# Kernel optimization log

Hardware: AMD Instinct MI355X
Metric: run time of the kernel (lower is better)

The kernel has to match this reference:

```python
import jax, jax.numpy as jnp
import numpy as np

B, S, D_MODEL, D_K = 4, 4096, 1024, 128
NEG = jnp.float32(-1e30)  # acts as -inf for masking; exp underflows to exactly 0 in fp32


def setup_inputs() -> dict:
    key = jax.random.key(0)
    ks = jax.random.split(key, 8)
    sc = 1.0 / np.sqrt(D_MODEL)
    x = jax.random.normal(ks[0], (B, S, D_MODEL), jnp.float32)
    padding_mask = (jax.random.uniform(ks[1], (B, S)) > 0.05).astype(jnp.float32)
    Wq = jax.random.normal(ks[2], (D_MODEL, D_K), jnp.float32) * sc
    bq = jax.random.normal(ks[3], (D_K,), jnp.float32) * 0.01
    Wk = jax.random.normal(ks[4], (D_MODEL, D_K), jnp.float32) * sc
    bk = jax.random.normal(ks[5], (D_K,), jnp.float32) * 0.01
    Wv = jax.random.normal(ks[6], (D_MODEL, D_K), jnp.float32) * sc
    bv = jax.random.normal(ks[7], (D_K,), jnp.float32) * 0.01
    return {"x": x, "padding_mask": padding_mask, "Wq": Wq, "bq": bq,
            "Wk": Wk, "bk": bk, "Wv": Wv, "bv": bv}


def reference(x, padding_mask, Wq, bq, Wk, bk, Wv, bv):
    # Self-attention path (enc_dec_layer_input is None), masked=True (causal).
    scale = jnp.sqrt(jnp.float32(Wq.shape[-1]))
    Q = x @ Wq + bq  # [B,S,Dk]
    K = x @ Wk + bk
    V = x @ Wv + bv
    scores = jnp.einsum('bqd,bkd->bqk', Q, K) / scale  # [B,S,S]
    # causal mask (torch: triu(1) filled with -inf) AND padding outer-product mask
    causal = jnp.tril(jnp.ones((S, S), dtype=bool))  # True = allowed
    pm = (padding_mask[:, :, None] * padding_mask[:, None, :]) > 0  # [B,S,S]
    allowed = causal[None] & pm
    scores = jnp.where(allowed, scores, NEG)
    attn = jax.nn.softmax(scores, axis=-1)
    # torch: fully-masked query rows give NaN -> nan_to_num -> 0.
    # A query row is dead iff its own token is padded (diagonal is causally allowed).
    row_alive = padding_mask > 0  # [B,S]
    attn = jnp.where(row_alive[:, :, None], attn, 0.0)
    out = jnp.einsum('bqk,bkd->bqd', attn, V)  # [B,S,Dk]
    return out
```

## Files before the change

### kernel.cpp

```cpp
#include <hip/hip_runtime.h>
#include <hip/hip_bf16.h>
#include <cstdint>

typedef __bf16 bf16x8 __attribute__((ext_vector_type(8)));
typedef float f32x4 __attribute__((ext_vector_type(4)));

#define MFMA16(a, b, c) __builtin_amdgcn_mfma_f32_16x16x32_bf16((a), (b), (c), 0, 0, 0)

__device__ __forceinline__ unsigned short f2bf(float f) {
  union { float f; unsigned u; } v; v.f = f;
  unsigned u = v.u;
  u += 0x7fffu + ((u >> 16) & 1u);
  return (unsigned short)(u >> 16);
}
__device__ __forceinline__ unsigned pk2(float a, float b) {
  __hip_bfloat162 h = __float22bfloat162_rn(make_float2(a, b));
  union { __hip_bfloat162 h; unsigned u; } v; v.h = h; return v.u;
}

__global__ __launch_bounds__(256) void convert_w(
    const float* __restrict__ Wq, const float* __restrict__ Wk,
    const float* __restrict__ Wv, unsigned short* __restrict__ wt) {
  int idx = blockIdx.x * 256 + threadIdx.x;
  int m = idx >> 17;
  int rem = idx & 131071;
  int k = rem >> 7;
  int n = rem & 127;
  const float* W = (m == 0) ? Wq : (m == 1) ? Wk : Wv;
  wt[(size_t)m * 131072 + (size_t)n * 1024 + k] = f2bf(W[(size_t)k * 128 + n]);
}

__global__ __launch_bounds__(512) void qkv_fused(
    const float* __restrict__ x, const unsigned short* __restrict__ wt_all,
    const float* __restrict__ bq, const float* __restrict__ bk,
    const float* __restrict__ bv,
    unsigned short* __restrict__ Qg, unsigned short* __restrict__ Kg,
    unsigned short* __restrict__ Vtg) {
  __shared__ unsigned short x_lds[64][40];
  __shared__ unsigned short w_lds[384][40];
  const int tid = threadIdx.x;
  const int lane = tid & 63;
  const int w = tid >> 6;
  const int m0 = blockIdx.x * 64;
  const int rh = w >> 2;
  const int cq = w & 3;
  const int lr = lane & 15;
  const int lk = (lane >> 4) * 8;

  f32x4 acc[2][6];
#pragma unroll
  for (int m = 0; m < 2; ++m)
#pragma unroll
    for (int n = 0; n < 6; ++n) acc[m][n] = (f32x4){0.f, 0.f, 0.f, 0.f};

  const int xr = tid >> 3;
  const int xc = (tid & 7) * 4;
  const float* xbase = x + (size_t)(m0 + xr) * 1024 + xc;
  const int j0 = tid, j1 = tid + 512, j2 = tid + 1024;
  const int wr0 = j0 >> 2, ws0 = (j0 & 3) * 8;
  const int wr1 = j1 >> 2, ws1 = (j1 & 3) * 8;
  const int wr2 = j2 >> 2, ws2 = (j2 & 3) * 8;
  const unsigned short* wp0 = wt_all + (size_t)wr0 * 1024 + ws0;
  const unsigned short* wp1 = wt_all + (size_t)wr1 * 1024 + ws1;
  const unsigned short* wp2 = wt_all + (size_t)wr2 * 1024 + ws2;

  float4 xA, xB;
  uint4 wA0, wA1, wA2, wB0, wB1, wB2;
  {
    xA = *(const float4*)xbase;
    wA0 = *(const uint4*)wp0; wA1 = *(const uint4*)wp1; wA2 = *(const uint4*)wp2;
    xB = *(const float4*)(xbase + 32);
    wB0 = *(const uint4*)(wp0 + 32); wB1 = *(const uint4*)(wp1 + 32); wB2 = *(const uint4*)(wp2 + 32);
  }

#define QKV_STORE(X, W0, W1, W2)                               \
  {                                                            \
    uint2 xw;                                                  \
    xw.x = pk2(X.x, X.y); xw.y = pk2(X.z, X.w);                \
    *(uint2*)&x_lds[xr][xc] = xw;                              \
    *(uint4*)&w_lds[wr0][ws0] = W0;                            \
    *(uint4*)&w_lds[wr1][ws1] = W1;                            \
    *(uint4*)&w_lds[wr2][ws2] = W2;                            \
  }

#define QKV_COMPUTE()                                          \
  {                                                            \
    bf16x8 af0 = *(const bf16x8*)&x_lds[rh * 32 + lr][lk];     \
    bf16x8 af1 = *(const bf16x8*)&x_lds[rh * 32 + 16 + lr][lk];\
    _Pragma("unroll")                                          \
    for (int n = 0; n < 6; ++n) {                              \
      bf16x8 bfv = *(const bf16x8*)&w_lds[cq * 96 + n * 16 + lr][lk]; \
      acc[0][n] = MFMA16(af0, bfv, acc[0][n]);                 \
      acc[1][n] = MFMA16(af1, bfv, acc[1][n]);                 \
    }                                                          \
  }

  for (int k0 = 0; k0 < 1024; k0 += 64) {
    __syncthreads();
    QKV_STORE(xA, wA0, wA1, wA2);
    __syncthreads();
    if (k0 + 64 < 1024) {
      xA = *(const float4*)(xbase + k0 + 64);
      wA0 = *(const uint4*)(wp0 + k0 + 64);
      wA1 = *(const uint4*)(wp1 + k0 + 64);
      wA2 = *(const uint4*)(wp2 + k0 + 64);
    }
    QKV_COMPUTE();
    __syncthreads();
    QKV_STORE(xB, wB0, wB1, wB2);
    __syncthreads();
    if (k0 + 96 < 1024) {
      xB = *(const float4*)(xbase + k0 + 96);
      wB0 = *(const uint4*)(wp0 + k0 + 96);
      wB1 = *(const uint4*)(wp1 + k0 + 96);
      wB2 = *(const uint4*)(wp2 + k0 + 96);
    }
    QKV_COMPUTE();
  }
#undef QKV_STORE
#undef QKV_COMPUTE

#pragma unroll
  for (int n = 0; n < 6; ++n) {
    const int gcol = cq * 96 + n * 16 + lr;
    const int mode = gcol >> 7;
    const int col = gcol & 127;
    const float bias = (mode == 0) ? bq[col] : (mode == 1) ? bk[col] : bv[col];
#pragma unroll
    for (int m = 0; m < 2; ++m)
#pragma unroll
      for (int r = 0; r < 4; ++r) {
        const int grow = m0 + rh * 32 + m * 16 + (lane >> 4) * 4 + r;
        float val = acc[m][n][r] + bias;
        if (mode == 0) {
          val *= 0.08838834764831845f;
          Qg[(size_t)grow * 128 + col] = f2bf(val);
        } else if (mode == 1) {
          Kg[(size_t)grow * 128 + col] = f2bf(val);
        } else {
          const int bb = grow >> 12, s = grow & 4095;
          Vtg[((size_t)bb * 128 + col) * 4096 + s] = f2bf(val);
        }
      }
  }
}

struct AttnLds {
  union {
    unsigned short K_lds[64][136];
    unsigned short P_lds[4][16][68];
  } u;
  unsigned short V_lds[128][72];
};

__device__ __forceinline__ void attn_tiles(
    AttnLds& S, const unsigned short* __restrict__ Kb,
    const unsigned short* __restrict__ Vb, const float* __restrict__ pmb,
    int q0, int tstart, int tend,
    const bf16x8 (&qf)[4], float& mrow, float& lsum, f32x4 (&o)[8]) {
  const int tid = threadIdx.x;
  const int lane = tid & 63;
  const int w = tid >> 6;
  const int lr = lane & 15;
  const int lg = lane >> 4;
  const int lk = lg * 8;
  const int q_own = q0 + w * 16 + lr;

  for (int t = tstart; t < tend; ++t) {
    const int k0 = t * 64;
    __syncthreads();
    {
      int kr = tid >> 2, seg = (tid & 3) * 32;
      const uint4* src = (const uint4*)(Kb + (size_t)(k0 + kr) * 128 + seg);
      uint4 v0 = src[0], v1 = src[1], v2 = src[2], v3 = src[3];
      uint4* dst = (uint4*)&S.u.K_lds[kr][seg];
      dst[0] = v0; dst[1] = v1; dst[2] = v2; dst[3] = v3;
      int d = tid >> 1, half = (tid & 1) * 32;
      const uint4* vs = (const uint4*)(Vb + (size_t)d * 4096 + k0 + half);
      uint4 u0 = vs[0], u1 = vs[1], u2 = vs[2], u3 = vs[3];
      uint4* vdst = (uint4*)&S.V_lds[d][half];
      vdst[0] = u0; vdst[1] = u1; vdst[2] = u2; vdst[3] = u3;
    }
    __syncthreads();

    f32x4 st[4];
#pragma unroll
    for (int f = 0; f < 4; ++f) {
      st[f] = (f32x4){0.f, 0.f, 0.f, 0.f};
#pragma unroll
      for (int dc = 0; dc < 4; ++dc) {
        bf16x8 kf = *(const bf16x8*)&S.u.K_lds[f * 16 + lr][dc * 32 + lk];
        st[f] = MFMA16(kf, qf[dc], st[f]);
      }
    }

    const unsigned long long mb = __ballot(pmb[k0 + lane] > 0.f);
    unsigned nib[4];
#pragma unroll
    for (int f = 0; f < 4; ++f) nib[f] = (unsigned)(mb >> (16 * f + 4 * lg)) & 0xFu;

    __syncthreads();

    float mx = -1e30f;
    if (k0 + 63 > q0 + (w << 4)) {
#pragma unroll
      for (int f = 0; f < 4; ++f)
#pragma unroll
        for (int r = 0; r < 4; ++r) {
          const bool ok = (((nib[f] >> r) & 1u) != 0u) &&
                          (k0 + 16 * f + 4 * lg + r <= q_own);
          const float s = ok ? st[f][r] : -1e30f;
          st[f][r] = s;
          mx = fmaxf(mx, s);
        }
    } else {
#pragma unroll
      for (int f = 0; f < 4; ++f)
#pragma unroll
        for (int r = 0; r < 4; ++r) {
          const bool ok = ((nib[f] >> r) & 1u) != 0u;
          const float s = ok ? st[f][r] : -1e30f;
          st[f][r] = s;
          mx = fmaxf(mx, s);
        }
    }
    mx = fmaxf(mx, __shfl_xor(mx, 16));
    mx = fmaxf(mx, __shfl_xor(mx, 32));
    const float mnew = fmaxf(mrow, mx);
    const float alpha = __expf(mrow - mnew);
    mrow = mnew;

    float sum = 0.f;
#pragma unroll
    for (int f = 0; f < 4; ++f) {
      const float p0 = (st[f][0] < -1e29f) ? 0.f : __expf(st[f][0] - mnew);
      const float p1 = (st[f][1] < -1e29f) ? 0.f : __expf(st[f][1] - mnew);
      const float p2 = (st[f][2] < -1e29f) ? 0.f : __expf(st[f][2] - mnew);
      const float p3 = (st[f][3] < -1e29f) ? 0.f : __expf(st[f][3] - mnew);
      sum += (p0 + p1) + (p2 + p3);
      uint2 u; u.x = pk2(p0, p1); u.y = pk2(p2, p3);
      *(uint2*)&S.u.P_lds[w][lr][16 * f + 4 * lg] = u;
    }
    sum += __shfl_xor(sum, 16);
    sum += __shfl_xor(sum, 32);
    lsum = lsum * alpha + sum;
#pragma unroll
    for (int n = 0; n < 8; ++n) o[n] *= alpha;

    __asm__ volatile("s_waitcnt lgkmcnt(0)" ::: "memory");
#pragma unroll
    for (int kc = 0; kc < 2; ++kc) {
      bf16x8 pa = *(const bf16x8*)&S.u.P_lds[w][lr][kc * 32 + lk];
#pragma unroll
      for (int n = 0; n < 8; ++n) {
        bf16x8 vf = *(const bf16x8*)&S.V_lds[n * 16 + lr][kc * 32 + lk];
        o[n] = MFMA16(vf, pa, o[n]);
      }
    }
  }
}

__global__ __launch_bounds__(256, 4) void attn_fwd(
    const unsigned short* __restrict__ Qg, const unsigned short* __restrict__ Kg,
    const unsigned short* __restrict__ Vtg, const float* __restrict__ pmask,
    float* __restrict__ out) {
  __shared__ AttnLds S;
  const int tid = threadIdx.x;
  const int lane = tid & 63;
  const int w = tid >> 6;
  const int b = blockIdx.y;
  const int q0 = blockIdx.x * 64;
  const int lr = lane & 15;
  const int lg = lane >> 4;
  const int lk = lg * 8;

  bf16x8 qf[4];
  {
    const unsigned short* qp = Qg + ((size_t)b * 4096 + q0 + w * 16 + lr) * 128;
#pragma unroll
    for (int dc = 0; dc < 4; ++dc) qf[dc] = *(const bf16x8*)(qp + dc * 32 + lk);
  }
  float mrow = -1e30f, lsum = 0.f;
  f32x4 o[8];
#pragma unroll
  for (int n = 0; n < 8; ++n) o[n] = (f32x4){0.f, 0.f, 0.f, 0.f};

  attn_tiles(S, Kg + (size_t)b * 4096 * 128, Vtg + (size_t)b * 128 * 4096,
             pmask + (size_t)b * 4096, q0, 0, (q0 >> 6) + 1, qf, mrow, lsum, o);

  const int qrow = q0 + w * 16 + lr;
  const bool alive = pmask[(size_t)b * 4096 + qrow] > 0.f;
  const float inv = (alive && lsum > 0.f) ? 1.f / lsum : 0.f;
  float* op = out + ((size_t)b * 4096 + qrow) * 128 + 4 * lg;
#pragma unroll
  for (int n = 0; n < 8; ++n) {
    f32x4 v = o[n] * inv;
    *(f32x4*)(op + n * 16) = v;
  }
}

__global__ __launch_bounds__(256, 4) void attn_split(
    const unsigned short* __restrict__ Qg, const unsigned short* __restrict__ Kg,
    const unsigned short* __restrict__ Vtg, const float* __restrict__ pmask,
    float* __restrict__ out, unsigned short* __restrict__ o_part,
    float* __restrict__ ml_part) {
  __shared__ AttnLds S;
  const int tid = threadIdx.x;
  const int lane = tid & 63;
  const int w = tid >> 6;
  const int L = blockIdx.x;
  const int xcd = L & 7;
  const int b = xcd >> 1;
  const int s = ((L >> 3) << 1) | (xcd & 1);
  int qb, c, nch;
  if (s < 8) {
    qb = s; c = 0; nch = 1;
  } else {
    int g = 1;
#pragma unroll
    for (int gg = 2; gg <= 7; ++gg)
      if (s >= 4 * gg * (gg + 1)) g = gg;
    const int rel = s - 4 * g * (g + 1);
    const int qq = rel / (g + 1);
    qb = 8 * g + qq;
    c = rel - qq * (g + 1);
    nch = g + 1;
  }
  const int q0 = qb * 64;
  const int tstart = c * 8;
  const int tend = min(c * 8 + 8, qb + 1);
  const int lr = lane & 15;
  const int lg = lane >> 4;
  const int lk = lg * 8;

  bf16x8 qf[4];
  {
    const unsigned short* qp = Qg + ((size_t)b * 4096 + q0 + w * 16 + lr) * 128;
#pragma unroll
    for (int dc = 0; dc < 4; ++dc) qf[dc] = *(const bf16x8*)(qp + dc * 32 + lk);
  }
  float mrow = -1e30f, lsum = 0.f;
  f32x4 o[8];
#pragma unroll
  for (int n = 0; n < 8; ++n) o[n] = (f32x4){0.f, 0.f, 0.f, 0.f};

  attn_tiles(S, Kg + (size_t)b * 4096 * 128, Vtg + (size_t)b * 128 * 4096,
             pmask + (size_t)b * 4096, q0, tstart, tend, qf, mrow, lsum, o);

  if (nch == 1) {
    const int qrow = q0 + w * 16 + lr;
    const bool alive = pmask[(size_t)b * 4096 + qrow] > 0.f;
    const float inv = (alive && lsum > 0.f) ? 1.f / lsum : 0.f;
    float* op = out + ((size_t)b * 4096 + qrow) * 128 + 4 * lg;
#pragma unroll
    for (int n = 0; n < 8; ++n) {
      f32x4 v = o[n] * inv;
      *(f32x4*)(op + n * 16) = v;
    }
  } else {
    const int slot = b * 280 + (s - 8);
    unsigned short* op = o_part + ((size_t)slot * 64 + w * 16 + lr) * 128 + 4 * lg;
#pragma unroll
    for (int n = 0; n < 8; ++n) {
      uint2 u; u.x = pk2(o[n][0], o[n][1]); u.y = pk2(o[n][2], o[n][3]);
      *(uint2*)(op + n * 16) = u;
    }
    if (lane < 16) {
      float* mp = ml_part + ((size_t)slot * 64 + w * 16 + lane) * 2;
      mp[0] = mrow;
      mp[1] = lsum;
    }
  }
}

__global__ __launch_bounds__(256) void attn_combine(
    const unsigned short* __restrict__ o_part, const float* __restrict__ ml_part,
    const float* __restrict__ pmask, float* __restrict__ out) {
  const int tid = threadIdx.x;
  const int lane = tid & 63;
  const int w = tid >> 6;
  const int g = blockIdx.x * 4 + w;
  const int b = g / 3584;
  const int rem = g % 3584;
  const int qb = 8 + (rem >> 6);
  const int row = rem & 63;
  const int qrow = qb * 64 + row;
  const int grp = qb >> 3;
  const int nch = grp + 1;
  const int pbase = b * 280 + 4 * grp * (grp + 1) - 8 + (qb - 8 * grp) * nch;

  float m[8], l[8];
  float M = -1e30f;
#pragma unroll
  for (int c = 0; c < 8; ++c)
    if (c < nch) {
      const float* mp = ml_part + ((size_t)(pbase + c) * 64 + row) * 2;
      m[c] = mp[0];
      l[c] = mp[1];
      M = fmaxf(M, m[c]);
    }
  float L = 0.f, wgt[8];
#pragma unroll
  for (int c = 0; c < 8; ++c)
    if (c < nch) {
      wgt[c] = __expf(m[c] - M);
      L += wgt[c] * l[c];
    }
  float2 acc = {0.f, 0.f};
#pragma unroll
  for (int c = 0; c < 8; ++c)
    if (c < nch) {
      const unsigned u = *(const unsigned*)(o_part + ((size_t)(pbase + c) * 64 + row) * 128 + lane * 2);
      acc.x += wgt[c] * __uint_as_float(u << 16);
      acc.y += wgt[c] * __uint_as_float(u & 0xffff0000u);
    }
  const bool alive = pmask[(size_t)b * 4096 + qrow] > 0.f;
  const float inv = (alive && L > 0.f) ? 1.f / L : 0.f;
  float2* op = (float2*)(out + ((size_t)b * 4096 + qrow) * 128);
  op[lane] = make_float2(acc.x * inv, acc.y * inv);
}

extern "C" void kernel_launch(void* const* d_in, const int* in_sizes, int n_in,
                              void* d_out, int out_size, void* d_ws, size_t ws_size,
                              hipStream_t stream) {
  (void)in_sizes; (void)n_in; (void)out_size;
  const float* x  = (const float*)d_in[0];
  const float* pm = (const float*)d_in[1];
  const float* Wq = (const float*)d_in[2];
  const float* bq = (const float*)d_in[3];
  const float* Wk = (const float*)d_in[4];
  const float* bk = (const float*)d_in[5];
  const float* Wv = (const float*)d_in[6];
  const float* bv = (const float*)d_in[7];
  float* out = (float*)d_out;

  unsigned short* ws  = (unsigned short*)d_ws;
  unsigned short* wt  = ws;
  unsigned short* Qg  = ws + 393216;
  unsigned short* Kg  = Qg + 2097152;
  unsigned short* Vtg = Kg + 2097152;
  unsigned short* o_part = ws + 6684672;
  float* ml_part = (float*)(ws + 15859712);
  const size_t WS_NEED = 15859712u * 2u + 573440u;

  convert_w<<<1536, 256, 0, stream>>>(Wq, Wk, Wv, wt);
  qkv_fused<<<256, 512, 0, stream>>>(x, wt, bq, bk, bv, Qg, Kg, Vtg);
  if (ws_size >= WS_NEED) {
    attn_split<<<1152, 256, 0, stream>>>(Qg, Kg, Vtg, pm, out, o_part, ml_part);
    attn_combine<<<3584, 256, 0, stream>>>(o_part, ml_part, pm, out);
  } else {
    attn_fwd<<<dim3(64, 4), 256, 0, stream>>>(Qg, Kg, Vtg, pm, out);
  }
}
```

Measured before the change: 106.9 us.

## Load QKV weight fragments straight from global memory and halve the row tile

The fused QKV projection no longer stages the bf16 weight tile in shared memory. Each wave now reads its MFMA B-operand fragments directly from global memory (expected to hit L2, since the weights total 768KB). The row tile drops from 64 to 32 with 256-thread blocks and twice as many blocks, which cuts LDS traffic and use and adds more blocks to spread across CUs. In exchange each wave issues uncoalesced 16-byte global loads per MFMA, and weight reuse across waves within a block is lost.

```diff
diff --git a/kernel.cpp b/kernel.cpp
--- a/kernel.cpp
+++ b/kernel.cpp
@@ -30,20 +30,17 @@
   wt[(size_t)m * 131072 + (size_t)n * 1024 + k] = f2bf(W[(size_t)k * 128 + n]);
 }
 
-__global__ __launch_bounds__(512) void qkv_fused(
+__global__ __launch_bounds__(256) void qkv_fused(
     const float* __restrict__ x, const unsigned short* __restrict__ wt_all,
     const float* __restrict__ bq, const float* __restrict__ bk,
     const float* __restrict__ bv,
     unsigned short* __restrict__ Qg, unsigned short* __restrict__ Kg,
     unsigned short* __restrict__ Vtg) {
-  __shared__ unsigned short x_lds[64][40];
-  __shared__ unsigned short w_lds[384][40];
+  __shared__ unsigned short x_lds[32][40];
   const int tid = threadIdx.x;
   const int lane = tid & 63;
-  const int w = tid >> 6;
-  const int m0 = blockIdx.x * 64;
-  const int rh = w >> 2;
-  const int cq = w & 3;
+  const int cq = tid >> 6;
+  const int m0 = blockIdx.x * 32;
   const int lr = lane & 15;
   const int lk = (lane >> 4) * 8;
 
@@ -56,69 +53,47 @@
   const int xr = tid >> 3;
   const int xc = (tid & 7) * 4;
   const float* xbase = x + (size_t)(m0 + xr) * 1024 + xc;
-  const int j0 = tid, j1 = tid + 512, j2 = tid + 1024;
-  const int wr0 = j0 >> 2, ws0 = (j0 & 3) * 8;
-  const int wr1 = j1 >> 2, ws1 = (j1 & 3) * 8;
-  const int wr2 = j2 >> 2, ws2 = (j2 & 3) * 8;
-  const unsigned short* wp0 = wt_all + (size_t)wr0 * 1024 + ws0;
-  const unsigned short* wp1 = wt_all + (size_t)wr1 * 1024 + ws1;
-  const unsigned short* wp2 = wt_all + (size_t)wr2 * 1024 + ws2;
-
-  float4 xA, xB;
-  uint4 wA0, wA1, wA2, wB0, wB1, wB2;
-  {
-    xA = *(const float4*)xbase;
-    wA0 = *(const uint4*)wp0; wA1 = *(const uint4*)wp1; wA2 = *(const uint4*)wp2;
-    xB = *(const float4*)(xbase + 32);
-    wB0 = *(const uint4*)(wp0 + 32); wB1 = *(const uint4*)(wp1 + 32); wB2 = *(const uint4*)(wp2 + 32);
-  }
-
-#define QKV_STORE(X, W0, W1, W2)                               \
-  {                                                            \
-    uint2 xw;                                                  \
-    xw.x = pk2(X.x, X.y); xw.y = pk2(X.z, X.w);                \
-    *(uint2*)&x_lds[xr][xc] = xw;                              \
-    *(uint4*)&w_lds[wr0][ws0] = W0;                            \
-    *(uint4*)&w_lds[wr1][ws1] = W1;                            \
-    *(uint4*)&w_lds[wr2][ws2] = W2;                            \
-  }
-
-#define QKV_COMPUTE()                                          \
-  {                                                            \
-    bf16x8 af0 = *(const bf16x8*)&x_lds[rh * 32 + lr][lk];     \
-    bf16x8 af1 = *(const bf16x8*)&x_lds[rh * 32 + 16 + lr][lk];\
-    _Pragma("unroll")                                          \
-    for (int n = 0; n < 6; ++n) {                              \
-      bf16x8 bfv = *(const bf16x8*)&w_lds[cq * 96 + n * 16 + lr][lk]; \
-      acc[0][n] = MFMA16(af0, bfv, acc[0][n]);                 \
-      acc[1][n] = MFMA16(af1, bfv, acc[1][n]);                 \
-    }                                                          \
-  }
+  const unsigned short* wbase = wt_all + (size_t)(cq * 96 + lr) * 1024 + lk;
+
+  float4 xA = *(const float4*)xbase;
+  float4 xB = *(const float4*)(xbase + 32);
 
   for (int k0 = 0; k0 < 1024; k0 += 64) {
     __syncthreads();
-    QKV_STORE(xA, wA0, wA1, wA2);
-    __syncthreads();
-    if (k0 + 64 < 1024) {
-      xA = *(const float4*)(xbase + k0 + 64);
-      wA0 = *(const uint4*)(wp0 + k0 + 64);
-      wA1 = *(const uint4*)(wp1 + k0 + 64);
-      wA2 = *(const uint4*)(wp2 + k0 + 64);
-    }
-    QKV_COMPUTE();
-    __syncthreads();
-    QKV_STORE(xB, wB0, wB1, wB2);
-    __syncthreads();
-    if (k0 + 96 < 1024) {
-      xB = *(const float4*)(xbase + k0 + 96);
-      wB0 = *(const uint4*)(wp0 + k0 + 96);
-      wB1 = *(const uint4*)(wp1 + k0 + 96);
-      wB2 = *(const uint4*)(wp2 + k0 + 96);
-    }
-    QKV_COMPUTE();
-  }
-#undef QKV_STORE
-#undef QKV_COMPUTE
+    {
+      uint2 xw; xw.x = pk2(xA.x, xA.y); xw.y = pk2(xA.z, xA.w);
+      *(uint2*)&x_lds[xr][xc] = xw;
+    }
+    __syncthreads();
+    if (k0 + 64 < 1024) xA = *(const float4*)(xbase + k0 + 64);
+    {
+      bf16x8 af0 = *(const bf16x8*)&x_lds[lr][lk];
+      bf16x8 af1 = *(const bf16x8*)&x_lds[16 + lr][lk];
+#pragma unroll
+      for (int n = 0; n < 6; ++n) {
+        bf16x8 bfr = *(const bf16x8*)(wbase + (size_t)n * 16384 + k0);
+        acc[0][n] = MFMA16(af0, bfr, acc[0][n]);
+        acc[1][n] = MFMA16(af1, bfr, acc[1][n]);
+      }
+    }
+    __syncthreads();
+    {
+      uint2 xw; xw.x = pk2(xB.x, xB.y); xw.y = pk2(xB.z, xB.w);
+      *(uint2*)&x_lds[xr][xc] = xw;
+    }
+    __syncthreads();
+    if (k0 + 96 < 1024) xB = *(const float4*)(xbase + k0 + 96);
+    {
+      bf16x8 af0 = *(const bf16x8*)&x_lds[lr][lk];
+      bf16x8 af1 = *(const bf16x8*)&x_lds[16 + lr][lk];
+#pragma unroll
+      for (int n = 0; n < 6; ++n) {
+        bf16x8 bfr = *(const bf16x8*)(wbase + (size_t)n * 16384 + k0 + 32);
+        acc[0][n] = MFMA16(af0, bfr, acc[0][n]);
+        acc[1][n] = MFMA16(af1, bfr, acc[1][n]);
+      }
+    }
+  }
 
 #pragma unroll
   for (int n = 0; n < 6; ++n) {
@@ -130,7 +105,7 @@
     for (int m = 0; m < 2; ++m)
 #pragma unroll
       for (int r = 0; r < 4; ++r) {
-        const int grow = m0 + rh * 32 + m * 16 + (lane >> 4) * 4 + r;
+        const int grow = m0 + m * 16 + (lane >> 4) * 4 + r;
         float val = acc[m][n][r] + bias;
         if (mode == 0) {
           val *= 0.08838834764831845f;
@@ -444,7 +419,7 @@
   const size_t WS_NEED = 15859712u * 2u + 573440u;
 
   convert_w<<<1536, 256, 0, stream>>>(Wq, Wk, Wv, wt);
-  qkv_fused<<<256, 512, 0, stream>>>(x, wt, bq, bk, bv, Qg, Kg, Vtg);
+  qkv_fused<<<512, 256, 0, stream>>>(x, wt, bq, bk, bv, Qg, Kg, Vtg);
   if (ws_size >= WS_NEED) {
     attn_split<<<1152, 256, 0, stream>>>(Qg, Kg, Vtg, pm, out, o_part, ml_part);
     attn_combine<<<3584, 256, 0, stream>>>(o_part, ml_part, pm, out);
```

Measured after the change: 133.7 us. 1.25x slower.
